# Kernel tuning notes

Measured on AMD Instinct MI355X. Metric: run time of the kernel, lower is better.

The kernel has to match this reference:

```python
import jax, jax.numpy as jnp
import numpy as np

N = 100000      # nodes
E = 1600000     # edges (avg degree 16)
D = 64          # in_channels == conv widths == lin width
G = 64          # graphs in batch
OUT = 10        # out_channels


def setup_inputs() -> dict:
    key = jax.random.key(0)
    ks = jax.random.split(key, 20)
    s = 0.1
    inp = {
        "x": jax.random.normal(ks[0], (N, D), jnp.float32),
        "edge_index": jax.random.randint(ks[1], (2, E), 0, N, dtype=jnp.int64),
        "batch": jnp.sort(jax.random.randint(ks[2], (N,), 0, G, dtype=jnp.int64)),
    }
    k = 3
    for i in range(3):  # 3 SAGEConv layers: lin_l (Wl, bl) on aggregated, lin_r (Wr, no bias) on root
        inp[f"c{i}_Wl"] = jax.random.normal(ks[k], (D, D), jnp.float32) * s; k += 1
        inp[f"c{i}_bl"] = jnp.zeros((D,), jnp.float32)
        inp[f"c{i}_Wr"] = jax.random.normal(ks[k], (D, D), jnp.float32) * s; k += 1
    inp["l0_W"] = jax.random.normal(ks[k], (D, D), jnp.float32) * s; k += 1
    inp["l0_b"] = jnp.zeros((D,), jnp.float32)
    inp["out_W"] = jax.random.normal(ks[k], (D, OUT), jnp.float32) * s; k += 1
    inp["out_b"] = jnp.zeros((OUT,), jnp.float32)
    return inp


def reference(x, edge_index, batch,
              c0_Wl, c0_bl, c0_Wr,
              c1_Wl, c1_bl, c1_Wr,
              c2_Wl, c2_bl, c2_Wr,
              l0_W, l0_b, out_W, out_b):
    src, dst = edge_index[0], edge_index[1]
    # in-degree of each target node (mean conv aggregation), computed once
    deg = jax.ops.segment_sum(jnp.ones((E,), x.dtype), dst, num_segments=N)
    inv_deg = (1.0 / jnp.maximum(deg, 1.0))[:, None]

    def sage(h, Wl, bl, Wr):
        # gather source features, mean-aggregate at targets, then lin_l(agg) + lin_r(h)
        agg = jax.ops.segment_sum(h[src], dst, num_segments=N) * inv_deg
        return agg @ Wl + bl + h @ Wr

    h = jax.nn.relu(sage(x, c0_Wl, c0_bl, c0_Wr))
    h = jax.nn.relu(sage(h, c1_Wl, c1_bl, c1_Wr))
    h = jax.nn.relu(sage(h, c2_Wl, c2_bl, c2_Wr))

    # global mean pool over graphs
    cnt = jax.ops.segment_sum(jnp.ones((N,), h.dtype), batch, num_segments=G)
    g = jax.ops.segment_sum(h, batch, num_segments=G) / jnp.maximum(cnt, 1.0)[:, None]

    g = jax.nn.relu(g @ l0_W + l0_b)
    return g @ out_W + out_b  # [G, OUT]
```

## Files before the change

### kernel.cpp

```cpp
#include <hip/hip_runtime.h>
#include <hip/hip_fp16.h>

#define WPB 8
#define PADK 136
#define BSH 8
#define BNODES 256
#define SC_BLOCKS 256
#define HIST_BLOCKS 256
#define HSTRIDE 512

typedef _Float16 half8 __attribute__((ext_vector_type(8)));
typedef _Float16 half4v __attribute__((ext_vector_type(4)));
typedef float floatx4 __attribute__((ext_vector_type(4)));

__global__ __launch_bounds__(256) void gnn_pre(const int* __restrict__ dst,
                                               int* __restrict__ bkt_cnt, int nbkt, int E,
                                               const int* __restrict__ batch,
                                               float* __restrict__ gcnt, int N,
                                               const float4* __restrict__ xin,
                                               ushort4* __restrict__ x16o, int n4,
                                               __half* __restrict__ x16,
                                               __half* __restrict__ hA,
                                               __half* __restrict__ hB,
                                               int* __restrict__ hist_all) {
    int tid = threadIdx.x;
    if (blockIdx.x < HIST_BLOCKS) {
        __shared__ int h[512];
        __shared__ int gb[64];
        for (int i = tid; i < nbkt; i += 256) h[i] = 0;
        if (tid < 64) gb[tid] = 0;
        __syncthreads();
        const int stride = HIST_BLOCKS * 256;
        for (int e = blockIdx.x * 256 + tid; e < E; e += stride)
            atomicAdd(&h[dst[e] >> BSH], 1);
        for (int i = blockIdx.x * 256 + tid; i < N; i += stride)
            atomicAdd(&gb[batch[i]], 1);
        __syncthreads();
        for (int i = tid; i < nbkt; i += 256) {
            int v = h[i];
            hist_all[blockIdx.x * HSTRIDE + i] = v;
            if (v) atomicAdd(&bkt_cnt[i], v);
        }
        if (tid < 64) {
            int v = gb[tid];
            if (v) atomicAdd(&gcnt[tid], (float)v);
        }
        if (blockIdx.x == 0 && tid < 64) {
            x16[(size_t)N * 64 + tid] = __ushort_as_half((unsigned short)0);
            hA[(size_t)N * 64 + tid] = __ushort_as_half((unsigned short)0);
            hB[(size_t)N * 64 + tid] = __ushort_as_half((unsigned short)0);
        }
    } else {
        int i = (blockIdx.x - HIST_BLOCKS) * 256 + tid;
        if (i < n4) {
            float4 f = xin[i];
            ushort4 o;
            o.x = __half_as_ushort(__float2half(f.x));
            o.y = __half_as_ushort(__float2half(f.y));
            o.z = __half_as_ushort(__float2half(f.z));
            o.w = __half_as_ushort(__float2half(f.w));
            x16o[i] = o;
        }
    }
}

__global__ void gnn_bkt_scan(const int* __restrict__ bkt_cnt, int* __restrict__ bkt_base,
                             int* __restrict__ row_ptr, int nbkt, int N) {
    int lane = threadIdx.x;
    int carry = 0;
    for (int base = 0; base < nbkt; base += 64) {
        int idx = base + lane;
        int v = (idx < nbkt) ? bkt_cnt[idx] : 0;
        int x = v;
#pragma unroll
        for (int off = 1; off < 64; off <<= 1) {
            int y = __shfl_up(x, off);
            if (lane >= off) x += y;
        }
        if (idx < nbkt) bkt_base[idx] = carry + (x - v);
        carry += __shfl(x, 63);
    }
    if (lane == 0) {
        bkt_base[nbkt] = carry;
        row_ptr[N] = carry;
    }
}

__global__ __launch_bounds__(256) void gnn_scan2(const int* __restrict__ hist_all,
                                                 const int* __restrict__ bkt_base,
                                                 int* __restrict__ blk_base_all, int nbkt) {
    int b = blockIdx.x;
    int t = threadIdx.x, lane = t & 63, wv = t >> 6;
    __shared__ int wsum[4];
    int v = hist_all[t * HSTRIDE + b];
    int x = v;
#pragma unroll
    for (int off = 1; off < 64; off <<= 1) {
        int y = __shfl_up(x, off);
        if (lane >= off) x += y;
    }
    if (lane == 63) wsum[wv] = x;
    __syncthreads();
    int wexcl = 0;
    for (int w = 0; w < wv; w++) wexcl += wsum[w];
    blk_base_all[t * HSTRIDE + b] = bkt_base[b] + wexcl + (x - v);
}

__global__ __launch_bounds__(256) void gnn_bkt_scatter(const int* __restrict__ src,
                                                       const int* __restrict__ dst,
                                                       const int* __restrict__ blk_base_all,
                                                       unsigned int* __restrict__ pairs,
                                                       int E, int nbkt) {
    __shared__ int cur[512];
    int tid = threadIdx.x;
    for (int i = tid; i < nbkt; i += 256) cur[i] = blk_base_all[blockIdx.x * HSTRIDE + i];
    __syncthreads();
    const int stride = SC_BLOCKS * 256;
    for (int e = blockIdx.x * 256 + tid; e < E; e += stride) {
        int d = dst[e];
        int b = d >> BSH;
        int p = atomicAdd(&cur[b], 1);
        pairs[p] = (unsigned int)src[e] | ((unsigned int)(d & (BNODES - 1)) << 24);
    }
}

__global__ __launch_bounds__(256) void gnn_bkt_csr(const unsigned int* __restrict__ pairs,
                                                   const int* __restrict__ bkt_base,
                                                   int* __restrict__ row_ptr,
                                                   float* __restrict__ inv_deg,
                                                   int* __restrict__ csr_src, int N) {
    __shared__ int hist[BNODES];
    __shared__ int excl[BNODES];
    __shared__ int cur[BNODES];
    int b = blockIdx.x;
    int base = bkt_base[b];
    int cnt = bkt_base[b + 1] - base;
    int nd0 = b << BSH;
    int tid = threadIdx.x;
    hist[tid] = 0;
    __syncthreads();
    for (int i = tid; i < cnt; i += 256) atomicAdd(&hist[pairs[base + i] >> 24], 1);
    __syncthreads();
    if (tid < 64) {
        int carry = 0;
#pragma unroll
        for (int c = 0; c < BNODES; c += 64) {
            int v = hist[c + tid];
            int x = v;
#pragma unroll
            for (int off = 1; off < 64; off <<= 1) {
                int y = __shfl_up(x, off);
                if (tid >= off) x += y;
            }
            excl[c + tid] = carry + (x - v);
            carry += __shfl(x, 63);
        }
    }
    __syncthreads();
    {
        int node = nd0 + tid;
        if (node < N) {
            row_ptr[node] = base + excl[tid];
            int d = hist[tid];
            inv_deg[node] = 1.0f / (float)(d > 1 ? d : 1);
        }
        cur[tid] = excl[tid];
    }
    __syncthreads();
    for (int i = tid; i < cnt; i += 256) {
        unsigned int u = pairs[base + i];
        int j = u >> 24;
        int pos = atomicAdd(&cur[j], 1);
        csr_src[base + pos] = (int)(u & 0xFFFFFFu);
    }
}

#define GATHC(eReg, i0, accum)                                  \
    {                                                           \
        int sj_ = __shfl(eReg, (i0) + quad);                    \
        half4v h_ = hin4v[(size_t)sj_ * 16 + m16];              \
        accum.x += (float)h_[0];                                \
        accum.y += (float)h_[1];                                \
        accum.z += (float)h_[2];                                \
        accum.w += (float)h_[3];                                \
    }

#define GATH16C(eReg, c0, accum)    \
    GATHC(eReg, (c0), accum);       \
    GATHC(eReg, (c0) + 4, accum);   \
    GATHC(eReg, (c0) + 8, accum);   \
    GATHC(eReg, (c0) + 12, accum);

__global__ __launch_bounds__(512, 4) void gnn_sage(const __half* __restrict__ hin,
                                                   __half* __restrict__ hout,
                                                   const int* __restrict__ row_ptr,
                                                   const int* __restrict__ csr_src,
                                                   const float* __restrict__ inv_deg,
                                                   const float* __restrict__ Wl,
                                                   const float* __restrict__ bl,
                                                   const float* __restrict__ Wr, int n) {
    __shared__ _Float16 w_lds[64 * PADK];
    __shared__ _Float16 in_lds[WPB][16 * PADK];
    int tid = threadIdx.x, lane = tid & 63, wv = tid >> 6;
    for (int i = tid; i < 64 * 64; i += 512) {
        int k = i >> 6, nn = i & 63;
        w_lds[nn * PADK + k] = (_Float16)Wl[i];
        w_lds[nn * PADK + 64 + k] = (_Float16)Wr[i];
    }
    __syncthreads();
    int ngroups = (n + 15) >> 4;
    int g = blockIdx.x * WPB + wv;
    if (g >= ngroups) return;
    int m16 = lane & 15, quad = lane >> 4;
    int hf = lane >> 5, col = lane & 31;
    float bias[4];
#pragma unroll
    for (int nt = 0; nt < 4; nt++) bias[nt] = bl[nt * 16 + m16];
    _Float16* my_in = in_lds[wv];
    const unsigned* hin32 = (const unsigned*)hin;
    const half4v* hin4v = (const half4v*)hin;
    int nd0 = g << 4;
    int nclamp = n - 1 - nd0;
    int idx = nd0 + lane;
    int rr = (lane <= 16) ? row_ptr[min(idx, n)] : 0;
    float ig = (lane < 16) ? inv_deg[min(idx, n - 1)] : 0.0f;

#pragma unroll
    for (int jp = 0; jp < 8; jp++) {
        int j2 = jp << 1;
        int nd = nd0 + min(j2 + hf, nclamp);
        unsigned u = hin32[(size_t)nd * 32 + col];
        ((unsigned*)(my_in + (j2 + hf) * PADK + 64))[col] = u;
    }

    int ef[16];
#pragma unroll
    for (int j = 0; j < 16; j++) {
        int jj = min(j, nclamp);
        int s0 = __shfl(rr, jj), s1 = __shfl(rr, jj + 1);
        int cb = min(64, s1 - s0);
        ef[j] = (lane < cb) ? csr_src[s0 + lane] : n;
    }

#pragma unroll
    for (int jp = 0; jp < 8; jp++) {
        int j2 = jp << 1;
        int jjA = min(j2, nclamp), jjB = min(j2 + 1, nclamp);
        int s0A = __shfl(rr, jjA), s1A = __shfl(rr, jjA + 1);
        int s0B = __shfl(rr, jjB), s1B = __shfl(rr, jjB + 1);
        float idgA = __shfl(ig, jjA), idgB = __shfl(ig, jjB);
        int cbA = min(64, s1A - s0A), cbB = min(64, s1B - s0B);
        floatx4 accA = {0.f, 0.f, 0.f, 0.f};
        floatx4 accB = {0.f, 0.f, 0.f, 0.f};
        GATH16C(ef[j2], 0, accA);
        GATH16C(ef[j2 + 1], 0, accB);
        if (cbA > 16) {
            GATH16C(ef[j2], 16, accA);
            if (cbA > 32) { GATH16C(ef[j2], 32, accA); }
            if (cbA > 48) { GATH16C(ef[j2], 48, accA); }
        }
        if (cbB > 16) {
            GATH16C(ef[j2 + 1], 16, accB);
            if (cbB > 32) { GATH16C(ef[j2 + 1], 32, accB); }
            if (cbB > 48) { GATH16C(ef[j2 + 1], 48, accB); }
        }
        for (int base = s0A + 64; base < s1A; base += 64) {
            int cb = min(64, s1A - base);
            int ei = (lane < cb) ? csr_src[base + lane] : n;
            for (int i0 = 0; i0 < cb; i0 += 16) { GATH16C(ei, i0, accA); }
        }
        for (int base = s0B + 64; base < s1B; base += 64) {
            int cb = min(64, s1B - base);
            int ei = (lane < cb) ? csr_src[base + lane] : n;
            for (int i0 = 0; i0 < cb; i0 += 16) { GATH16C(ei, i0, accB); }
        }
        accA.x += __shfl_xor(accA.x, 16); accA.y += __shfl_xor(accA.y, 16);
        accA.z += __shfl_xor(accA.z, 16); accA.w += __shfl_xor(accA.w, 16);
        accA.x += __shfl_xor(accA.x, 32); accA.y += __shfl_xor(accA.y, 32);
        accA.z += __shfl_xor(accA.z, 32); accA.w += __shfl_xor(accA.w, 32);
        accB.x += __shfl_xor(accB.x, 16); accB.y += __shfl_xor(accB.y, 16);
        accB.z += __shfl_xor(accB.z, 16); accB.w += __shfl_xor(accB.w, 16);
        accB.x += __shfl_xor(accB.x, 32); accB.y += __shfl_xor(accB.y, 32);
        accB.z += __shfl_xor(accB.z, 32); accB.w += __shfl_xor(accB.w, 32);
        if (quad == 0) {
            half4v hw;
            hw[0] = (_Float16)(accA.x * idgA);
            hw[1] = (_Float16)(accA.y * idgA);
            hw[2] = (_Float16)(accA.z * idgA);
            hw[3] = (_Float16)(accA.w * idgA);
            *(half4v*)(my_in + j2 * PADK + m16 * 4) = hw;
        } else if (quad == 1) {
            half4v hw;
            hw[0] = (_Float16)(accB.x * idgB);
            hw[1] = (_Float16)(accB.y * idgB);
            hw[2] = (_Float16)(accB.z * idgB);
            hw[3] = (_Float16)(accB.w * idgB);
            *(half4v*)(my_in + (j2 + 1) * PADK + m16 * 4) = hw;
        }
    }
    half8 afrag[4];
    const _Float16* abase = my_in + m16 * PADK + quad * 8;
#pragma unroll
    for (int ks = 0; ks < 4; ks++) afrag[ks] = *(const half8*)(abase + ks * 32);
    floatx4 accv[4];
#pragma unroll
    for (int nt = 0; nt < 4; nt++) {
        accv[nt].x = 0.f; accv[nt].y = 0.f; accv[nt].z = 0.f; accv[nt].w = 0.f;
    }
#pragma unroll
    for (int nt = 0; nt < 4; nt++) {
        const _Float16* bbase = w_lds + (nt * 16 + m16) * PADK + quad * 8;
#pragma unroll
        for (int ks = 0; ks < 4; ks++) {
            half8 bfrag = *(const half8*)(bbase + ks * 32);
            accv[nt] = __builtin_amdgcn_mfma_f32_16x16x32_f16(afrag[ks], bfrag, accv[nt], 0, 0, 0);
        }
    }
#pragma unroll
    for (int nt = 0; nt < 4; nt++) {
#pragma unroll
        for (int r = 0; r < 4; r++) {
            int node = nd0 + quad * 4 + r;
            if (node < n) {
                float v = fmaxf(accv[nt][r] + bias[nt], 0.0f);
                hout[(size_t)node * 64 + nt * 16 + m16] = __float2half(v);
            }
        }
    }
}

__global__ __launch_bounds__(512, 4) void gnn_sage_pool(const __half* __restrict__ hin,
                                                        const int* __restrict__ row_ptr,
                                                        const int* __restrict__ csr_src,
                                                        const float* __restrict__ inv_deg,
                                                        const float* __restrict__ Wl,
                                                        const float* __restrict__ bl,
                                                        const float* __restrict__ Wr,
                                                        const int* __restrict__ batch,
                                                        float* __restrict__ gsum, int n) {
    __shared__ _Float16 w_lds[64 * PADK];
    __shared__ _Float16 in_lds[WPB][16 * PADK];
    int tid = threadIdx.x, lane = tid & 63, wv = tid >> 6;
    for (int i = tid; i < 64 * 64; i += 512) {
        int k = i >> 6, nn = i & 63;
        w_lds[nn * PADK + k] = (_Float16)Wl[i];
        w_lds[nn * PADK + 64 + k] = (_Float16)Wr[i];
    }
    __syncthreads();
    int ngroups = (n + 15) >> 4;
    int g = blockIdx.x * WPB + wv;
    if (g >= ngroups) return;
    int m16 = lane & 15, quad = lane >> 4;
    int hf = lane >> 5, col = lane & 31;
    float bias[4];
#pragma unroll
    for (int nt = 0; nt < 4; nt++) bias[nt] = bl[nt * 16 + m16];
    _Float16* my_in = in_lds[wv];
    const unsigned* hin32 = (const unsigned*)hin;
    const half4v* hin4v = (const half4v*)hin;
    int nd0 = g << 4;
    int nclamp = n - 1 - nd0;
    int idx = nd0 + lane;
    int rr = (lane <= 16) ? row_ptr[min(idx, n)] : 0;
    float ig = (lane < 16) ? inv_deg[min(idx, n - 1)] : 0.0f;

#pragma unroll
    for (int jp = 0; jp < 8; jp++) {
        int j2 = jp << 1;
        int nd = nd0 + min(j2 + hf, nclamp);
        unsigned u = hin32[(size_t)nd * 32 + col];
        ((unsigned*)(my_in + (j2 + hf) * PADK + 64))[col] = u;
    }

    int ef[16];
#pragma unroll
    for (int j = 0; j < 16; j++) {
        int jj = min(j, nclamp);
        int s0 = __shfl(rr, jj), s1 = __shfl(rr, jj + 1);
        int cb = min(64, s1 - s0);
        ef[j] = (lane < cb) ? csr_src[s0 + lane] : n;
    }

#pragma unroll
    for (int jp = 0; jp < 8; jp++) {
        int j2 = jp << 1;
        int jjA = min(j2, nclamp), jjB = min(j2 + 1, nclamp);
        int s0A = __shfl(rr, jjA), s1A = __shfl(rr, jjA + 1);
        int s0B = __shfl(rr, jjB), s1B = __shfl(rr, jjB + 1);
        float idgA = __shfl(ig, jjA), idgB = __shfl(ig, jjB);
        int cbA = min(64, s1A - s0A), cbB = min(64, s1B - s0B);
        floatx4 accA = {0.f, 0.f, 0.f, 0.f};
        floatx4 accB = {0.f, 0.f, 0.f, 0.f};
        GATH16C(ef[j2], 0, accA);
        GATH16C(ef[j2 + 1], 0, accB);
        if (cbA > 16) {
            GATH16C(ef[j2], 16, accA);
            if (cbA > 32) { GATH16C(ef[j2], 32, accA); }
            if (cbA > 48) { GATH16C(ef[j2], 48, accA); }
        }
        if (cbB > 16) {
            GATH16C(ef[j2 + 1], 16, accB);
            if (cbB > 32) { GATH16C(ef[j2 + 1], 32, accB); }
            if (cbB > 48) { GATH16C(ef[j2 + 1], 48, accB); }
        }
        for (int base = s0A + 64; base < s1A; base += 64) {
            int cb = min(64, s1A - base);
            int ei = (lane < cb) ? csr_src[base + lane] : n;
            for (int i0 = 0; i0 < cb; i0 += 16) { GATH16C(ei, i0, accA); }
        }
        for (int base = s0B + 64; base < s1B; base += 64) {
            int cb = min(64, s1B - base);
            int ei = (lane < cb) ? csr_src[base + lane] : n;
            for (int i0 = 0; i0 < cb; i0 += 16) { GATH16C(ei, i0, accB); }
        }
        accA.x += __shfl_xor(accA.x, 16); accA.y += __shfl_xor(accA.y, 16);
        accA.z += __shfl_xor(accA.z, 16); accA.w += __shfl_xor(accA.w, 16);
        accA.x += __shfl_xor(accA.x, 32); accA.y += __shfl_xor(accA.y, 32);
        accA.z += __shfl_xor(accA.z, 32); accA.w += __shfl_xor(accA.w, 32);
        accB.x += __shfl_xor(accB.x, 16); accB.y += __shfl_xor(accB.y, 16);
        accB.z += __shfl_xor(accB.z, 16); accB.w += __shfl_xor(accB.w, 16);
        accB.x += __shfl_xor(accB.x, 32); accB.y += __shfl_xor(accB.y, 32);
        accB.z += __shfl_xor(accB.z, 32); accB.w += __shfl_xor(accB.w, 32);
        if (quad == 0) {
            half4v hw;
            hw[0] = (_Float16)(accA.x * idgA);
            hw[1] = (_Float16)(accA.y * idgA);
            hw[2] = (_Float16)(accA.z * idgA);
            hw[3] = (_Float16)(accA.w * idgA);
            *(half4v*)(my_in + j2 * PADK + m16 * 4) = hw;
        } else if (quad == 1) {
            half4v hw;
            hw[0] = (_Float16)(accB.x * idgB);
            hw[1] = (_Float16)(accB.y * idgB);
            hw[2] = (_Float16)(accB.z * idgB);
            hw[3] = (_Float16)(accB.w * idgB);
            *(half4v*)(my_in + (j2 + 1) * PADK + m16 * 4) = hw;
        }
    }
    half8 afrag[4];
    const _Float16* abase = my_in + m16 * PADK + quad * 8;
#pragma unroll
    for (int ks = 0; ks < 4; ks++) afrag[ks] = *(const half8*)(abase + ks * 32);
    floatx4 accv[4];
#pragma unroll
    for (int nt = 0; nt < 4; nt++) {
        accv[nt].x = 0.f; accv[nt].y = 0.f; accv[nt].z = 0.f; accv[nt].w = 0.f;
    }
#pragma unroll
    for (int nt = 0; nt < 4; nt++) {
        const _Float16* bbase = w_lds + (nt * 16 + m16) * PADK + quad * 8;
#pragma unroll
        for (int ks = 0; ks < 4; ks++) {
            half8 bfrag = *(const half8*)(bbase + ks * 32);
            accv[nt] = __builtin_amdgcn_mfma_f32_16x16x32_f16(afrag[ks], bfrag, accv[nt], 0, 0, 0);
        }
    }
    int bFirst = batch[nd0];
    int bLast = batch[min(nd0 + 15, n - 1)];
    if (bFirst == bLast && nd0 + 15 < n) {
#pragma unroll
        for (int nt = 0; nt < 4; nt++) {
            float s = fmaxf(accv[nt][0] + bias[nt], 0.0f) + fmaxf(accv[nt][1] + bias[nt], 0.0f) +
                      fmaxf(accv[nt][2] + bias[nt], 0.0f) + fmaxf(accv[nt][3] + bias[nt], 0.0f);
            s += __shfl_xor(s, 16);
            s += __shfl_xor(s, 32);
            if (quad == 0) atomicAdd(&gsum[bFirst * 64 + nt * 16 + m16], s);
        }
    } else {
#pragma unroll
        for (int nt = 0; nt < 4; nt++) {
#pragma unroll
            for (int r = 0; r < 4; r++) {
                int node = nd0 + quad * 4 + r;
                if (node < n) {
                    int bg = batch[node];
                    float v = fmaxf(accv[nt][r] + bias[nt], 0.0f);
                    atomicAdd(&gsum[bg * 64 + nt * 16 + m16], v);
                }
            }
        }
    }
}

__global__ __launch_bounds__(256) void gnn_head(const float* __restrict__ gsum,
                                                const float* __restrict__ gcnt,
                                                const float* __restrict__ l0W,
                                                const float* __restrict__ l0b,
                                                const float* __restrict__ outW,
                                                const float* __restrict__ outb,
                                                float* __restrict__ out, int G, int OUT) {
    __shared__ float gm[64 * 64];
    __shared__ float t2[64 * 64];
    int tid = threadIdx.x;
    for (int i = tid; i < G * 64; i += 256) {
        int r = i >> 6;
        gm[i] = gsum[i] / fmaxf(gcnt[r], 1.0f);
    }
    __syncthreads();
    for (int i = tid; i < G * 64; i += 256) {
        int r = i >> 6, c = i & 63;
        float s = l0b[c];
#pragma unroll 8
        for (int k = 0; k < 64; k++) s += gm[(r << 6) + k] * l0W[(k << 6) + c];
        t2[i] = fmaxf(s, 0.0f);
    }
    __syncthreads();
    for (int i = tid; i < G * OUT; i += 256) {
        int r = i / OUT, c = i - r * OUT;
        float s = outb[c];
#pragma unroll 8
        for (int k = 0; k < 64; k++) s += t2[(r << 6) + k] * outW[k * OUT + c];
        out[i] = s;
    }
}

extern "C" void kernel_launch(void* const* d_in, const int* in_sizes, int n_in,
                              void* d_out, int out_size, void* d_ws, size_t ws_size,
                              hipStream_t stream) {
    const float* x = (const float*)d_in[0];
    const int* ei = (const int*)d_in[1];
    const int* batch = (const int*)d_in[2];
    const float* Wl[3] = {(const float*)d_in[3], (const float*)d_in[6], (const float*)d_in[9]};
    const float* bl[3] = {(const float*)d_in[4], (const float*)d_in[7], (const float*)d_in[10]};
    const float* Wr[3] = {(const float*)d_in[5], (const float*)d_in[8], (const float*)d_in[11]};
    const float* l0W = (const float*)d_in[12];
    const float* l0b = (const float*)d_in[13];
    const float* outW = (const float*)d_in[14];
    const float* outb = (const float*)d_in[15];

    int N = in_sizes[2];
    int E = in_sizes[1] / 2;
    int OUT = 10;
    int G = out_size / OUT;
    const int* src = ei;
    const int* dst = ei + E;
    int NBKT = (N + BNODES - 1) >> BSH;

    char* ws = (char*)d_ws;
    size_t off = 0;
    auto alloc = [&](size_t b) -> char* {
        char* p = ws + off;
        off = (off + b + 255) & ~(size_t)255;
        return p;
    };
    int* row_ptr = (int*)alloc((size_t)(N + 1) * 4);
    int* csr_src = (int*)alloc((size_t)E * 4);
    float* inv_deg = (float*)alloc((size_t)N * 4);
    size_t zoff = off;
    int* bkt_cnt = (int*)alloc((size_t)NBKT * 4);
    float* gcnt = (float*)alloc((size_t)G * 4);
    float* gsum = (float*)alloc((size_t)G * 64 * 4);
    size_t zlen = off - zoff;
    int* bkt_base = (int*)alloc((size_t)(NBKT + 1) * 4);
    int* hist_all = (int*)alloc((size_t)HIST_BLOCKS * HSTRIDE * 4);
    int* blk_base_all = (int*)alloc((size_t)HIST_BLOCKS * HSTRIDE * 4);
    unsigned int* pairs = (unsigned int*)alloc((size_t)E * 4);
    __half* x16 = (__half*)alloc((size_t)(N + 1) * 64 * 2);
    __half* hA = (__half*)alloc((size_t)(N + 1) * 64 * 2);
    __half* hB = (__half*)alloc((size_t)(N + 1) * 64 * 2);

    hipMemsetAsync(ws + zoff, 0, zlen, stream);

    int n4 = N * 64 / 4;
    int pre_blocks = HIST_BLOCKS + (n4 + 255) / 256;
    gnn_pre<<<pre_blocks, 256, 0, stream>>>(dst, bkt_cnt, NBKT, E, batch, gcnt, N,
                                            (const float4*)x, (ushort4*)x16, n4,
                                            x16, hA, hB, hist_all);
    gnn_bkt_scan<<<1, 64, 0, stream>>>(bkt_cnt, bkt_base, row_ptr, NBKT, N);
    gnn_scan2<<<NBKT, 256, 0, stream>>>(hist_all, bkt_base, blk_base_all, NBKT);
    gnn_bkt_scatter<<<SC_BLOCKS, 256, 0, stream>>>(src, dst, blk_base_all, pairs, E, NBKT);
    gnn_bkt_csr<<<NBKT, 256, 0, stream>>>(pairs, bkt_base, row_ptr, inv_deg, csr_src, N);

    int ngroups = (N + 15) >> 4;
    int sage_blocks = (ngroups + WPB - 1) / WPB;
    gnn_sage<<<sage_blocks, 512, 0, stream>>>(x16, hA, row_ptr, csr_src, inv_deg,
                                              Wl[0], bl[0], Wr[0], N);
    gnn_sage<<<sage_blocks, 512, 0, stream>>>(hA, hB, row_ptr, csr_src, inv_deg,
                                              Wl[1], bl[1], Wr[1], N);
    gnn_sage_pool<<<sage_blocks, 512, 0, stream>>>(hB, row_ptr, csr_src, inv_deg,
                                                   Wl[2], bl[2], Wr[2], batch, gsum, N);

    gnn_head<<<1, 256, 0, stream>>>(gsum, gcnt, l0W, l0b, outW, outb, (float*)d_out, G, OUT);
}
```

Before: 312.7 us.

## Vectorize edge loads in CSR build, batch gather loads, widen head block

The histogram, bucket scatter and per-bucket CSR kernels now read dst/src/pairs as 4-wide vectors, handling alignment prologue and epilogue, to cut load instruction count. The SAGE gather macros are restructured so four gathered rows are loaded before accumulation, exposing more memory-level parallelism. The head kernel runs with 1024 threads instead of 256. Changes in atomic order alter the CSR edge order but not the sums beyond rounding; the vector casts assume 16-byte alignment of the index arrays.

Measured after the change: 293.5 us. -6.1%, faster.

```diff
diff --git a/kernel.cpp b/kernel.cpp
--- a/kernel.cpp
+++ b/kernel.cpp
@@ -31,8 +31,20 @@
         if (tid < 64) gb[tid] = 0;
         __syncthreads();
         const int stride = HIST_BLOCKS * 256;
-        for (int e = blockIdx.x * 256 + tid; e < E; e += stride)
-            atomicAdd(&h[dst[e] >> BSH], 1);
+        if ((E & 3) == 0) {
+            const int4* dst4 = (const int4*)dst;
+            int E4 = E >> 2;
+            for (int e = blockIdx.x * 256 + tid; e < E4; e += stride) {
+                int4 d = dst4[e];
+                atomicAdd(&h[d.x >> BSH], 1);
+                atomicAdd(&h[d.y >> BSH], 1);
+                atomicAdd(&h[d.z >> BSH], 1);
+                atomicAdd(&h[d.w >> BSH], 1);
+            }
+        } else {
+            for (int e = blockIdx.x * 256 + tid; e < E; e += stride)
+                atomicAdd(&h[dst[e] >> BSH], 1);
+        }
         for (int i = blockIdx.x * 256 + tid; i < N; i += stride)
             atomicAdd(&gb[batch[i]], 1);
         __syncthreads();
@@ -116,11 +128,29 @@
     for (int i = tid; i < nbkt; i += 256) cur[i] = blk_base_all[blockIdx.x * HSTRIDE + i];
     __syncthreads();
     const int stride = SC_BLOCKS * 256;
-    for (int e = blockIdx.x * 256 + tid; e < E; e += stride) {
-        int d = dst[e];
-        int b = d >> BSH;
-        int p = atomicAdd(&cur[b], 1);
-        pairs[p] = (unsigned int)src[e] | ((unsigned int)(d & (BNODES - 1)) << 24);
+    if ((E & 3) == 0) {
+        const int4* dst4 = (const int4*)dst;
+        const int4* src4 = (const int4*)src;
+        int E4 = E >> 2;
+        for (int e = blockIdx.x * 256 + tid; e < E4; e += stride) {
+            int4 d = dst4[e];
+            int4 s = src4[e];
+            int p0 = atomicAdd(&cur[d.x >> BSH], 1);
+            pairs[p0] = (unsigned int)s.x | ((unsigned int)(d.x & (BNODES - 1)) << 24);
+            int p1 = atomicAdd(&cur[d.y >> BSH], 1);
+            pairs[p1] = (unsigned int)s.y | ((unsigned int)(d.y & (BNODES - 1)) << 24);
+            int p2 = atomicAdd(&cur[d.z >> BSH], 1);
+            pairs[p2] = (unsigned int)s.z | ((unsigned int)(d.z & (BNODES - 1)) << 24);
+            int p3 = atomicAdd(&cur[d.w >> BSH], 1);
+            pairs[p3] = (unsigned int)s.w | ((unsigned int)(d.w & (BNODES - 1)) << 24);
+        }
+    } else {
+        for (int e = blockIdx.x * 256 + tid; e < E; e += stride) {
+            int d = dst[e];
+            int b = d >> BSH;
+            int p = atomicAdd(&cur[b], 1);
+            pairs[p] = (unsigned int)src[e] | ((unsigned int)(d & (BNODES - 1)) << 24);
+        }
     }
 }
 
@@ -139,7 +169,22 @@
     int tid = threadIdx.x;
     hist[tid] = 0;
     __syncthreads();
-    for (int i = tid; i < cnt; i += 256) atomicAdd(&hist[pairs[base + i] >> 24], 1);
+    {
+        int a0 = (4 - (base & 3)) & 3;
+        a0 = min(a0, cnt);
+        for (int i = tid; i < a0; i += 256) atomicAdd(&hist[pairs[base + i] >> 24], 1);
+        int vcnt = (cnt - a0) >> 2;
+        const uint4* p4 = (const uint4*)(pairs + base + a0);
+        for (int i = tid; i < vcnt; i += 256) {
+            uint4 u = p4[i];
+            atomicAdd(&hist[u.x >> 24], 1);
+            atomicAdd(&hist[u.y >> 24], 1);
+            atomicAdd(&hist[u.z >> 24], 1);
+            atomicAdd(&hist[u.w >> 24], 1);
+        }
+        for (int i = a0 + (vcnt << 2) + tid; i < cnt; i += 256)
+            atomicAdd(&hist[pairs[base + i] >> 24], 1);
+    }
     __syncthreads();
     if (tid < 64) {
         int carry = 0;
@@ -167,29 +212,47 @@
         cur[tid] = excl[tid];
     }
     __syncthreads();
-    for (int i = tid; i < cnt; i += 256) {
-        unsigned int u = pairs[base + i];
-        int j = u >> 24;
-        int pos = atomicAdd(&cur[j], 1);
-        csr_src[base + pos] = (int)(u & 0xFFFFFFu);
-    }
-}
-
-#define GATHC(eReg, i0, accum)                                  \
-    {                                                           \
-        int sj_ = __shfl(eReg, (i0) + quad);                    \
-        half4v h_ = hin4v[(size_t)sj_ * 16 + m16];              \
-        accum.x += (float)h_[0];                                \
-        accum.y += (float)h_[1];                                \
-        accum.z += (float)h_[2];                                \
-        accum.w += (float)h_[3];                                \
-    }
-
-#define GATH16C(eReg, c0, accum)    \
-    GATHC(eReg, (c0), accum);       \
-    GATHC(eReg, (c0) + 4, accum);   \
-    GATHC(eReg, (c0) + 8, accum);   \
-    GATHC(eReg, (c0) + 12, accum);
+    {
+        int a0 = (4 - (base & 3)) & 3;
+        a0 = min(a0, cnt);
+        for (int i = tid; i < a0; i += 256) {
+            unsigned int u = pairs[base + i];
+            int pos = atomicAdd(&cur[u >> 24], 1);
+            csr_src[base + pos] = (int)(u & 0xFFFFFFu);
+        }
+        int vcnt = (cnt - a0) >> 2;
+        const uint4* p4 = (const uint4*)(pairs + base + a0);
+        for (int i = tid; i < vcnt; i += 256) {
+            uint4 u = p4[i];
+            int pos0 = atomicAdd(&cur[u.x >> 24], 1);
+            csr_src[base + pos0] = (int)(u.x & 0xFFFFFFu);
+            int pos1 = atomicAdd(&cur[u.y >> 24], 1);
+            csr_src[base + pos1] = (int)(u.y & 0xFFFFFFu);
+            int pos2 = atomicAdd(&cur[u.z >> 24], 1);
+            csr_src[base + pos2] = (int)(u.z & 0xFFFFFFu);
+            int pos3 = atomicAdd(&cur[u.w >> 24], 1);
+            csr_src[base + pos3] = (int)(u.w & 0xFFFFFFu);
+        }
+        for (int i = a0 + (vcnt << 2) + tid; i < cnt; i += 256) {
+            unsigned int u = pairs[base + i];
+            int pos = atomicAdd(&cur[u >> 24], 1);
+            csr_src[base + pos] = (int)(u & 0xFFFFFFu);
+        }
+    }
+}
+
+#define LOAD4(eReg, c0, vArr)                                  \
+    _Pragma("unroll") for (int c_ = 0; c_ < 4; c_++) {         \
+        int sj_ = __shfl(eReg, (c0) + c_ * 4 + quad);          \
+        vArr[c_] = hin4v[(size_t)sj_ * 16 + m16];              \
+    }
+#define ACC4(vArr, accum)                                      \
+    _Pragma("unroll") for (int c_ = 0; c_ < 4; c_++) {         \
+        accum.x += (float)vArr[c_][0];                         \
+        accum.y += (float)vArr[c_][1];                         \
+        accum.z += (float)vArr[c_][2];                         \
+        accum.w += (float)vArr[c_][3];                         \
+    }
 
 __global__ __launch_bounds__(512, 4) void gnn_sage(const __half* __restrict__ hin,
                                                    __half* __restrict__ hout,
@@ -252,27 +315,44 @@
         int cbA = min(64, s1A - s0A), cbB = min(64, s1B - s0B);
         floatx4 accA = {0.f, 0.f, 0.f, 0.f};
         floatx4 accB = {0.f, 0.f, 0.f, 0.f};
-        GATH16C(ef[j2], 0, accA);
-        GATH16C(ef[j2 + 1], 0, accB);
+        {
+            half4v vA[4], vB[4];
+            LOAD4(ef[j2], 0, vA);
+            LOAD4(ef[j2 + 1], 0, vB);
+            ACC4(vA, accA);
+            ACC4(vB, accB);
+        }
         if (cbA > 16) {
-            GATH16C(ef[j2], 16, accA);
-            if (cbA > 32) { GATH16C(ef[j2], 32, accA); }
-            if (cbA > 48) { GATH16C(ef[j2], 48, accA); }
+            half4v v0[4];
+            LOAD4(ef[j2], 16, v0);
+            ACC4(v0, accA);
+            if (cbA > 32) { half4v v1[4]; LOAD4(ef[j2], 32, v1); ACC4(v1, accA); }
+            if (cbA > 48) { half4v v2[4]; LOAD4(ef[j2], 48, v2); ACC4(v2, accA); }
         }
         if (cbB > 16) {
-            GATH16C(ef[j2 + 1], 16, accB);
-            if (cbB > 32) { GATH16C(ef[j2 + 1], 32, accB); }
-            if (cbB > 48) { GATH16C(ef[j2 + 1], 48, accB); }
-        }
-        for (int base = s0A + 64; base < s1A; base += 64) {
-            int cb = min(64, s1A - base);
-            int ei = (lane < cb) ? csr_src[base + lane] : n;
-            for (int i0 = 0; i0 < cb; i0 += 16) { GATH16C(ei, i0, accA); }
-        }
-        for (int base = s0B + 64; base < s1B; base += 64) {
-            int cb = min(64, s1B - base);
-            int ei = (lane < cb) ? csr_src[base + lane] : n;
-            for (int i0 = 0; i0 < cb; i0 += 16) { GATH16C(ei, i0, accB); }
+            half4v v0[4];
+            LOAD4(ef[j2 + 1], 16, v0);
+            ACC4(v0, accB);
+            if (cbB > 32) { half4v v1[4]; LOAD4(ef[j2 + 1], 32, v1); ACC4(v1, accB); }
+            if (cbB > 48) { half4v v2[4]; LOAD4(ef[j2 + 1], 48, v2); ACC4(v2, accB); }
+        }
+        for (int base_ = s0A + 64; base_ < s1A; base_ += 64) {
+            int cb = min(64, s1A - base_);
+            int ei = (lane < cb) ? csr_src[base_ + lane] : n;
+            for (int i0 = 0; i0 < cb; i0 += 16) {
+                half4v vt[4];
+                LOAD4(ei, i0, vt);
+                ACC4(vt, accA);
+            }
+        }
+        for (int base_ = s0B + 64; base_ < s1B; base_ += 64) {
+            int cb = min(64, s1B - base_);
+            int ei = (lane < cb) ? csr_src[base_ + lane] : n;
+            for (int i0 = 0; i0 < cb; i0 += 16) {
+                half4v vt[4];
+                LOAD4(ei, i0, vt);
+                ACC4(vt, accB);
+            }
         }
         accA.x += __shfl_xor(accA.x, 16); accA.y += __shfl_xor(accA.y, 16);
         accA.z += __shfl_xor(accA.z, 16); accA.w += __shfl_xor(accA.w, 16);
@@ -391,27 +471,44 @@
         int cbA = min(64, s1A - s0A), cbB = min(64, s1B - s0B);
         floatx4 accA = {0.f, 0.f, 0.f, 0.f};
         floatx4 accB = {0.f, 0.f, 0.f, 0.f};
-        GATH16C(ef[j2], 0, accA);
-        GATH16C(ef[j2 + 1], 0, accB);
+        {
+            half4v vA[4], vB[4];
+            LOAD4(ef[j2], 0, vA);
+            LOAD4(ef[j2 + 1], 0, vB);
+            ACC4(vA, accA);
+            ACC4(vB, accB);
+        }
         if (cbA > 16) {
-            GATH16C(ef[j2], 16, accA);
-            if (cbA > 32) { GATH16C(ef[j2], 32, accA); }
-            if (cbA > 48) { GATH16C(ef[j2], 48, accA); }
+            half4v v0[4];
+            LOAD4(ef[j2], 16, v0);
+            ACC4(v0, accA);
+            if (cbA > 32) { half4v v1[4]; LOAD4(ef[j2], 32, v1); ACC4(v1, accA); }
+            if (cbA > 48) { half4v v2[4]; LOAD4(ef[j2], 48, v2); ACC4(v2, accA); }
         }
         if (cbB > 16) {
-            GATH16C(ef[j2 + 1], 16, accB);
-            if (cbB > 32) { GATH16C(ef[j2 + 1], 32, accB); }
-            if (cbB > 48) { GATH16C(ef[j2 + 1], 48, accB); }
-        }
-        for (int base = s0A + 64; base < s1A; base += 64) {
-            int cb = min(64, s1A - base);
-            int ei = (lane < cb) ? csr_src[base + lane] : n;
-            for (int i0 = 0; i0 < cb; i0 += 16) { GATH16C(ei, i0, accA); }
-        }
-        for (int base = s0B + 64; base < s1B; base += 64) {
-            int cb = min(64, s1B - base);
-            int ei = (lane < cb) ? csr_src[base + lane] : n;
-            for (int i0 = 0; i0 < cb; i0 += 16) { GATH16C(ei, i0, accB); }
+            half4v v0[4];
+            LOAD4(ef[j2 + 1], 16, v0);
+            ACC4(v0, accB);
+            if (cbB > 32) { half4v v1[4]; LOAD4(ef[j2 + 1], 32, v1); ACC4(v1, accB); }
+            if (cbB > 48) { half4v v2[4]; LOAD4(ef[j2 + 1], 48, v2); ACC4(v2, accB); }
+        }
+        for (int base_ = s0A + 64; base_ < s1A; base_ += 64) {
+            int cb = min(64, s1A - base_);
+            int ei = (lane < cb) ? csr_src[base_ + lane] : n;
+            for (int i0 = 0; i0 < cb; i0 += 16) {
+                half4v vt[4];
+                LOAD4(ei, i0, vt);
+                ACC4(vt, accA);
+            }
+        }
+        for (int base_ = s0B + 64; base_ < s1B; base_ += 64) {
+            int cb = min(64, s1B - base_);
+            int ei = (lane < cb) ? csr_src[base_ + lane] : n;
+            for (int i0 = 0; i0 < cb; i0 += 16) {
+                half4v vt[4];
+                LOAD4(ei, i0, vt);
+                ACC4(vt, accB);
+            }
         }
         accA.x += __shfl_xor(accA.x, 16); accA.y += __shfl_xor(accA.y, 16);
         accA.z += __shfl_xor(accA.z, 16); accA.w += __shfl_xor(accA.w, 16);
@@ -482,22 +579,22 @@
     }
 }
 
-__global__ __launch_bounds__(256) void gnn_head(const float* __restrict__ gsum,
-                                                const float* __restrict__ gcnt,
-                                                const float* __restrict__ l0W,
-                                                const float* __restrict__ l0b,
-                                                const float* __restrict__ outW,
-                                                const float* __restrict__ outb,
-                                                float* __restrict__ out, int G, int OUT) {
+__global__ __launch_bounds__(1024) void gnn_head(const float* __restrict__ gsum,
+                                                 const float* __restrict__ gcnt,
+                                                 const float* __restrict__ l0W,
+                                                 const float* __restrict__ l0b,
+                                                 const float* __restrict__ outW,
+                                                 const float* __restrict__ outb,
+                                                 float* __restrict__ out, int G, int OUT) {
     __shared__ float gm[64 * 64];
     __shared__ float t2[64 * 64];
     int tid = threadIdx.x;
-    for (int i = tid; i < G * 64; i += 256) {
+    for (int i = tid; i < G * 64; i += 1024) {
         int r = i >> 6;
         gm[i] = gsum[i] / fmaxf(gcnt[r], 1.0f);
     }
     __syncthreads();
-    for (int i = tid; i < G * 64; i += 256) {
+    for (int i = tid; i < G * 64; i += 1024) {
         int r = i >> 6, c = i & 63;
         float s = l0b[c];
 #pragma unroll 8
@@ -505,7 +602,7 @@
         t2[i] = fmaxf(s, 0.0f);
     }
     __syncthreads();
-    for (int i = tid; i < G * OUT; i += 256) {
+    for (int i = tid; i < G * OUT; i += 1024) {
         int r = i / OUT, c = i - r * OUT;
         float s = outb[c];
 #pragma unroll 8
@@ -580,5 +677,5 @@
     gnn_sage_pool<<<sage_blocks, 512, 0, stream>>>(hB, row_ptr, csr_src, inv_deg,
                                                    Wl[2], bl[2], Wr[2], batch, gsum, N);
 
-    gnn_head<<<1, 256, 0, stream>>>(gsum, gcnt, l0W, l0b, outW, outb, (float*)d_out, G, OUT);
-}
+    gnn_head<<<1, 1024, 0, stream>>>(gsum, gcnt, l0W, l0b, outW, outb, (float*)d_out, G, OUT);
+}
```
